# Performance work log

Measured on AMD Instinct MI355X. Metric: run time of the kernel, lower is better.

## Reference

```python
import jax, jax.numpy as jnp
import numpy as np

B, IN_DIM, HIDDEN, N_CLASSES, D_Z = 16384, 1024, 2048, 8, 256
LN_EPS = 1e-5  # torch.nn.LayerNorm default


def _l2_normalize(x, axis=1, eps=1e-12):
    # matches F.normalize: x / max(||x||, eps)
    n = jnp.sqrt(jnp.sum(x * x, axis=axis, keepdims=True))
    return x / jnp.maximum(n, eps)


def setup_inputs() -> dict:
    key = jax.random.key(0)
    ks = jax.random.split(key, 9)
    s1 = 1.0 / np.sqrt(IN_DIM)
    s2 = 1.0 / np.sqrt(HIDDEN)
    return {
        "feat": jax.random.normal(ks[0], (B, IN_DIM), dtype=jnp.float32),
        "z_cat": jax.random.normal(ks[1], (B, D_Z), dtype=jnp.float32),
        "mu_cat": jax.random.normal(ks[2], (N_CLASSES, D_Z), dtype=jnp.float32),
        "ln_gamma": jnp.ones((N_CLASSES, IN_DIM), dtype=jnp.float32),
        "ln_beta": jnp.zeros((N_CLASSES, IN_DIM), dtype=jnp.float32),
        "W1": jax.random.uniform(ks[3], (N_CLASSES, IN_DIM, HIDDEN), jnp.float32, -s1, s1),
        "b1": jax.random.uniform(ks[4], (N_CLASSES, HIDDEN), jnp.float32, -s1, s1),
        "W2": jax.random.uniform(ks[5], (N_CLASSES, HIDDEN, N_CLASSES), jnp.float32, -s2, s2),
        "b2": jax.random.uniform(ks[6], (N_CLASSES, N_CLASSES), jnp.float32, -s2, s2),
        "tau_gate": 1,
    }


def reference(feat, z_cat, mu_cat, ln_gamma, ln_beta, W1, b1, W2, b2, tau_gate):
    # --- cosine-similarity softmax gate ---
    zn = _l2_normalize(z_cat, axis=1)            # [B, Dz]
    mun = _l2_normalize(mu_cat, axis=1)          # [E, Dz]
    sims = zn @ mun.T                            # [B, E]
    tau = max(1e-6, float(tau_gate))
    w = jax.nn.softmax(sims / tau, axis=1)       # [B, E]

    # --- batched experts: LN -> Linear -> ReLU -> (Dropout=identity, eval) -> Linear ---
    mu = jnp.mean(feat, axis=-1, keepdims=True)
    var = jnp.mean(jnp.square(feat - mu), axis=-1, keepdims=True)
    xhat = (feat - mu) * jax.lax.rsqrt(var + LN_EPS)            # [B, D] (shared)
    x_e = xhat[None] * ln_gamma[:, None, :] + ln_beta[:, None, :]  # [E, B, D]
    h = jax.nn.relu(jnp.einsum('ebd,edh->ebh', x_e, W1) + b1[:, None, :])  # [E, B, H]
    exp_logits = jnp.einsum('ebh,ehc->ebc', h, W2) + b2[:, None, :]        # [E, B, C]

    # --- gate-weighted sum over experts ---
    logits = jnp.einsum('ebc,be->bc', exp_logits, w)  # [B, C]
    return logits, w
```

## Files before the change

kernel.cpp:

```cpp
#include <hip/hip_runtime.h>
#include <hip/hip_bf16.h>
#include <cstdint>

#define NB     16384
#define DIN    1024
#define HID    2048
#define NE     8
#define NC     8
#define DZ     256

#define BK2    32
#define NKT    (DIN / BK2)
#define GRID_MAIN 256

typedef short bf16x8 __attribute__((ext_vector_type(8)));
typedef float f32x4  __attribute__((ext_vector_type(4)));

__device__ __forceinline__ unsigned short f2bf(float f) {
    unsigned int u = __float_as_uint(f);
    unsigned int r = (u + 0x7FFFu + ((u >> 16) & 1u)) >> 16;
    return (unsigned short)r;
}

__device__ __forceinline__ void async_copy16(const void* g, void* l) {
    __builtin_amdgcn_global_load_lds(
        (const __attribute__((address_space(1))) unsigned int*)g,
        (__attribute__((address_space(3))) unsigned int*)l, 16, 0, 0);
}

__global__ __launch_bounds__(256) void k_gate(const float* __restrict__ z,
                                              const float* __restrict__ mu,
                                              const int* __restrict__ tau_i,
                                              const float* __restrict__ b2,
                                              float* __restrict__ wout,
                                              float* __restrict__ logits) {
    int row = blockIdx.x * 4 + (threadIdx.x >> 6);
    int l = threadIdx.x & 63;
    float4 zv = *(const float4*)&z[(size_t)row * DZ + l * 4];
    float zz = zv.x * zv.x + zv.y * zv.y + zv.z * zv.z + zv.w * zv.w;
    float dots[NE], mm[NE];
#pragma unroll
    for (int e = 0; e < NE; ++e) {
        float4 m = *(const float4*)&mu[e * DZ + l * 4];
        dots[e] = zv.x * m.x + zv.y * m.y + zv.z * m.z + zv.w * m.w;
        mm[e]   = m.x * m.x + m.y * m.y + m.z * m.z + m.w * m.w;
    }
#pragma unroll
    for (int off = 32; off; off >>= 1) {
        zz += __shfl_xor(zz, off);
#pragma unroll
        for (int e = 0; e < NE; ++e) {
            dots[e] += __shfl_xor(dots[e], off);
            mm[e]   += __shfl_xor(mm[e], off);
        }
    }
    float zn = fmaxf(sqrtf(zz), 1e-12f);
    float tau = fmaxf(1e-6f, (float)tau_i[0]);
    float s[NE], mx = -1e30f;
#pragma unroll
    for (int e = 0; e < NE; ++e) {
        s[e] = dots[e] / (zn * fmaxf(sqrtf(mm[e]), 1e-12f)) / tau;
        mx = fmaxf(mx, s[e]);
    }
    float sum = 0.f;
#pragma unroll
    for (int e = 0; e < NE; ++e) { s[e] = expf(s[e] - mx); sum += s[e]; }
    float inv = 1.f / sum;
    if (l < NE) {
        wout[(size_t)row * NE + l] = s[l] * inv;
        float acc = 0.f;
#pragma unroll
        for (int e = 0; e < NE; ++e) acc += s[e] * inv * b2[e * NC + l];
        logits[(size_t)row * NC + l] = acc;
    }
}

__global__ __launch_bounds__(256) void k_ln(const float* __restrict__ feat,
                                            unsigned short* __restrict__ xhat) {
    int row = blockIdx.x;
    int t = threadIdx.x;
    float4 v = *(const float4*)&feat[(size_t)row * DIN + t * 4];
    float s  = v.x + v.y + v.z + v.w;
    float sq = v.x * v.x + v.y * v.y + v.z * v.z + v.w * v.w;
#pragma unroll
    for (int off = 32; off; off >>= 1) {
        s  += __shfl_down(s, off);
        sq += __shfl_down(sq, off);
    }
    __shared__ float ls[8];
    int w = t >> 6, l = t & 63;
    if (l == 0) { ls[w] = s; ls[4 + w] = sq; }
    __syncthreads();
    s  = ls[0] + ls[1] + ls[2] + ls[3];
    sq = ls[4] + ls[5] + ls[6] + ls[7];
    float mean = s * (1.f / DIN);
    float var  = sq * (1.f / DIN) - mean * mean;
    float r = 1.0f / sqrtf(var + 1e-5f);
    uint2 p;
    p.x = (unsigned)f2bf((v.x - mean) * r) | ((unsigned)f2bf((v.y - mean) * r) << 16);
    p.y = (unsigned)f2bf((v.z - mean) * r) | ((unsigned)f2bf((v.w - mean) * r) << 16);
    *(uint2*)&xhat[(size_t)row * DIN + t * 4] = p;
}

__global__ __launch_bounds__(256) void k_w2prep(const float* __restrict__ W2,
                                                const float* __restrict__ b1,
                                                unsigned short* __restrict__ w2t,
                                                float* __restrict__ b1p) {
    int i = blockIdx.x * 256 + threadIdx.x;
    int e = i >> 15;
    int rem = i & 32767;
    int c = rem >> 11;
    int h = rem & 2047;
    float v = (c < NC) ? W2[((size_t)(e * HID + h)) * NC + c] : 0.f;
    w2t[i] = f2bf(v);
    if (i < NE * HID) b1p[i] = b1[i];
}

__global__ __launch_bounds__(256) void k_w1prep(const float* __restrict__ W1,
                                                const float* __restrict__ gamma,
                                                const float* __restrict__ beta,
                                                unsigned short* __restrict__ w1t,
                                                float* __restrict__ b1p) {
    __shared__ float tile[64][65];
    int e  = blockIdx.z;
    int d0 = blockIdx.y * 64;
    int h0 = blockIdx.x * 64;
    int tx = threadIdx.x & 15, ty = threadIdx.x >> 4;
#pragma unroll
    for (int rr = 0; rr < 4; ++rr) {
        int d = ty + rr * 16;
        float4 v = *(const float4*)&W1[((size_t)e * DIN + d0 + d) * HID + h0 + tx * 4];
        tile[tx * 4 + 0][d] = v.x;
        tile[tx * 4 + 1][d] = v.y;
        tile[tx * 4 + 2][d] = v.z;
        tile[tx * 4 + 3][d] = v.w;
    }
    __syncthreads();
    float4 g = *(const float4*)&gamma[(size_t)e * DIN + d0 + tx * 4];
#pragma unroll
    for (int rr = 0; rr < 4; ++rr) {
        int h = ty + rr * 16;
        uint2 p;
        p.x = (unsigned)f2bf(tile[h][tx * 4 + 0] * g.x) |
              ((unsigned)f2bf(tile[h][tx * 4 + 1] * g.y) << 16);
        p.y = (unsigned)f2bf(tile[h][tx * 4 + 2] * g.z) |
              ((unsigned)f2bf(tile[h][tx * 4 + 3] * g.w) << 16);
        *(uint2*)&w1t[((size_t)e * HID + h0 + h) * DIN + d0 + tx * 4] = p;
    }
    if (threadIdx.x < 64) {
        int h = threadIdx.x;
        float sacc = 0.f;
        for (int r = 0; r < 64; ++r)
            sacc += beta[(size_t)e * DIN + d0 + r] * tile[h][r];
        atomicAdd(&b1p[(size_t)e * HID + h0 + h], sacc);
    }
}


#define WAITV(n_) asm volatile("s_waitcnt vmcnt(" #n_ ")" ::: "memory")
#define BAR()  do { __builtin_amdgcn_s_barrier(); __builtin_amdgcn_sched_barrier(0); } while (0)

#define STAGE(tile_) do {                                                     \
    char* dst_ = (char*)lds + (((tile_) & 3) << 15) + (t << 4);               \
    const size_t ro_ = (size_t)srow * DIN + (size_t)(tile_) * BK2 + sk;       \
    async_copy16(gA + ro_, dst_);                                             \
    async_copy16(gA + ro_ + (size_t)128 * DIN, dst_ + 8192);                  \
    async_copy16(gB + ro_, dst_ + 16384);                                     \
    async_copy16(gB + ro_ + (size_t)128 * DIN, dst_ + 24576);                 \
} while (0)

#define KBODY(kt_) do {                                                       \
    const short* la_ = (const short*)(lds + (((kt_) & 3) << 15));             \
    const short* lb_ = la_ + 8192;                                            \
    bf16x8 bF_[4];                                                            \
    _Pragma("unroll")                                                         \
    for (int j_ = 0; j_ < 4; ++j_)                                            \
        bF_[j_] = *(const bf16x8*)&lb_[(wn + 16 * j_ + ml) * BK2 + cswz];     \
    __builtin_amdgcn_s_setprio(1);                                            \
    _Pragma("unroll")                                                         \
    for (int i_ = 0; i_ < 8; ++i_) {                                          \
        const bf16x8 aF_ = *(const bf16x8*)&la_[(wm + 16 * i_ + ml) * BK2 + cswz]; \
        _Pragma("unroll")                                                     \
        for (int j_ = 0; j_ < 4; ++j_)                                        \
            acc[i_][j_] = __builtin_amdgcn_mfma_f32_16x16x32_bf16(            \
                aF_, bF_[j_], acc[i_][j_], 0, 0, 0);                          \
    }                                                                         \
    __builtin_amdgcn_s_setprio(0);                                            \
} while (0)

__global__ __launch_bounds__(512, 2) void moe_main(
        const unsigned short* __restrict__ xhat,
        const unsigned short* __restrict__ w1t,
        const float* __restrict__ b1p,
        const unsigned short* __restrict__ w2t,
        const float* __restrict__ wg,
        float* __restrict__ logits) {
    __shared__ __align__(16) char lds[131072];

    const int t  = threadIdx.x;
    const int w  = t >> 6, l = t & 63;
    const int q  = l >> 4, ml = l & 15;
    const int wm = (w >> 2) * 128;
    const int wn = (w & 3) * 64;
    const int cswz = (q ^ ((ml >> 1) & 3)) * 8;
    const int srow = t >> 2;
    const int sk   = ((t & 3) ^ ((srow >> 1) & 3)) * 8;

    const int e    = blockIdx.x & 7;
    const int slot = blockIdx.x >> 3;
    char* myht = (char*)lds + w * 5120;

    for (int pr = 0; pr < 2; ++pr) {
        const int b0 = (pr * 32 + slot) * 256;
        const unsigned short* gB = xhat + (size_t)b0 * DIN;

        f32x4 acc2[4];
#pragma unroll
        for (int tb = 0; tb < 4; ++tb) acc2[tb] = (f32x4){0.f, 0.f, 0.f, 0.f};

        for (int ms = 0; ms < 8; ++ms) {
            const int hid0 = ms * 256;
            const unsigned short* gA = w1t + ((size_t)e * HID + hid0) * DIN;

            f32x4 acc[8][4];
#pragma unroll
            for (int i = 0; i < 8; ++i)
#pragma unroll
                for (int j = 0; j < 4; ++j) acc[i][j] = (f32x4){0.f, 0.f, 0.f, 0.f};

            STAGE(0); STAGE(1); STAGE(2);
#pragma unroll 1
            for (int kt = 0; kt < NKT - 3; ++kt) {
                WAITV(8);
                BAR();
                STAGE(kt + 3);
                KBODY(kt);
            }
            WAITV(8); BAR(); KBODY(29);
            WAITV(4); BAR(); KBODY(30);
            WAITV(0); BAR(); KBODY(31);

#pragma unroll
            for (int s = 0; s < 4; ++s) {
#pragma unroll
                for (int i2 = 0; i2 < 2; ++i2) {
                    const int i = 2 * s + i2;
                    const float4 bias = *(const float4*)
                        &b1p[(size_t)e * HID + hid0 + wm + 16 * i + 4 * q];
#pragma unroll
                    for (int j = 0; j < 4; ++j) {
                        float v0 = fmaxf(acc[i][j].x + bias.x, 0.f);
                        float v1 = fmaxf(acc[i][j].y + bias.y, 0.f);
                        float v2 = fmaxf(acc[i][j].z + bias.z, 0.f);
                        float v3 = fmaxf(acc[i][j].w + bias.w, 0.f);
                        uint2 p;
                        p.x = (unsigned)f2bf(v0) | ((unsigned)f2bf(v1) << 16);
                        p.y = (unsigned)f2bf(v2) | ((unsigned)f2bf(v3) << 16);
                        *(uint2*)(myht + (16 * j + ml) * 80 + (16 * i2 + 4 * q) * 2) = p;
                    }
                }
                const bf16x8 b2f = *(const bf16x8*)&w2t[((size_t)e * 16 + ml) * HID +
                                                        hid0 + wm + 32 * s + 8 * q];
#pragma unroll
                for (int tb = 0; tb < 4; ++tb) {
                    const bf16x8 a2f =
                        *(const bf16x8*)(myht + (16 * tb + ml) * 80 + q * 16);
                    acc2[tb] = __builtin_amdgcn_mfma_f32_16x16x32_bf16(
                        a2f, b2f, acc2[tb], 0, 0, 0);
                }
            }
            __syncthreads();
        }

        float* red = (float*)(lds + 65536);
        if (w >= 4) {
            float* dst = red + ((w & 3) * 64 + l) * 16;
#pragma unroll
            for (int tb = 0; tb < 4; ++tb)
#pragma unroll
                for (int r = 0; r < 4; ++r) dst[tb * 4 + r] = acc2[tb][r];
        }
        __syncthreads();
        if (w < 4) {
            const float* src = red + (w * 64 + l) * 16;
            if (ml < NC) {
#pragma unroll
                for (int tb = 0; tb < 4; ++tb) {
#pragma unroll
                    for (int r = 0; r < 4; ++r) {
                        float v = acc2[tb][r] + src[tb * 4 + r];
                        const int bg = b0 + wn + 16 * tb + 4 * q + r;
                        atomicAdd(&logits[(size_t)bg * NC + ml],
                                  wg[(size_t)bg * NE + e] * v);
                    }
                }
            }
        }
        __syncthreads();
    }
}

extern "C" void kernel_launch(void* const* d_in, const int* in_sizes, int n_in,
                              void* d_out, int out_size, void* d_ws, size_t ws_size,
                              hipStream_t stream) {
    const float* feat  = (const float*)d_in[0];
    const float* z     = (const float*)d_in[1];
    const float* mu    = (const float*)d_in[2];
    const float* gamma = (const float*)d_in[3];
    const float* beta  = (const float*)d_in[4];
    const float* W1    = (const float*)d_in[5];
    const float* b1    = (const float*)d_in[6];
    const float* W2    = (const float*)d_in[7];
    const float* b2    = (const float*)d_in[8];
    const int*   tau   = (const int*)d_in[9];

    float* logits = (float*)d_out;
    float* wout   = logits + (size_t)NB * NC;

    char* ws = (char*)d_ws;
    unsigned short* xhat = (unsigned short*)ws;
    unsigned short* w1t  = (unsigned short*)(ws + 33554432);
    unsigned short* w2t  = (unsigned short*)(ws + 67108864);
    float*          b1p  = (float*)(ws + 67633152);

    k_gate<<<NB / 4, 256, 0, stream>>>(z, mu, tau, b2, wout, logits);
    k_ln<<<NB, 256, 0, stream>>>(feat, xhat);
    k_w2prep<<<(NE * 16 * HID) / 256, 256, 0, stream>>>(W2, b1, w2t, b1p);
    k_w1prep<<<dim3(HID / 64, DIN / 64, NE), 256, 0, stream>>>(W1, gamma, beta, w1t, b1p);
    moe_main<<<dim3(GRID_MAIN), 512, 0, stream>>>(xhat, w1t, b1p, w2t, wout, logits);
}
```

Before: 723.2 us.

## Split GEMM k-iteration into two phases with interleaved staging and barriers

Each k-tile iteration of the main GEMM loop now runs as two halves. Each half loads four A fragments into registers, issues half of the next tile's async global-to-LDS copies (A in the first half, B in the second), passes a barrier, then runs 16 MFMAs. This spreads memory issue across the compute phases and keeps waves in lockstep, in the style of ping-pong scheduling. It adds two extra workgroup barriers per iteration, which may cost more than the overlap gains.

```diff
diff --git a/kernel.cpp b/kernel.cpp
--- a/kernel.cpp
+++ b/kernel.cpp
@@ -160,31 +160,53 @@
 #define WAITV(n_) asm volatile("s_waitcnt vmcnt(" #n_ ")" ::: "memory")
 #define BAR()  do { __builtin_amdgcn_s_barrier(); __builtin_amdgcn_sched_barrier(0); } while (0)
 
-#define STAGE(tile_) do {                                                     \
+#define STAGEA(tile_) do {                                                    \
     char* dst_ = (char*)lds + (((tile_) & 3) << 15) + (t << 4);               \
-    const size_t ro_ = (size_t)srow * DIN + (size_t)(tile_) * BK2 + sk;       \
+    const size_t ro_ = rowoff + (size_t)(tile_) * BK2;                        \
     async_copy16(gA + ro_, dst_);                                             \
     async_copy16(gA + ro_ + (size_t)128 * DIN, dst_ + 8192);                  \
-    async_copy16(gB + ro_, dst_ + 16384);                                     \
-    async_copy16(gB + ro_ + (size_t)128 * DIN, dst_ + 24576);                 \
 } while (0)
 
-#define KBODY(kt_) do {                                                       \
+#define STAGEB(tile_) do {                                                    \
+    char* dst_ = (char*)lds + (((tile_) & 3) << 15) + 16384 + (t << 4);       \
+    const size_t ro_ = rowoff + (size_t)(tile_) * BK2;                        \
+    async_copy16(gB + ro_, dst_);                                             \
+    async_copy16(gB + ro_ + (size_t)128 * DIN, dst_ + 8192);                  \
+} while (0)
+
+#define ITER(kt_, DO_STAGE) do {                                              \
     const short* la_ = (const short*)(lds + (((kt_) & 3) << 15));             \
     const short* lb_ = la_ + 8192;                                            \
-    bf16x8 bF_[4];                                                            \
+    bf16x8 bF_[4], aF_[4];                                                    \
     _Pragma("unroll")                                                         \
     for (int j_ = 0; j_ < 4; ++j_)                                            \
         bF_[j_] = *(const bf16x8*)&lb_[(wn + 16 * j_ + ml) * BK2 + cswz];     \
+    _Pragma("unroll")                                                         \
+    for (int i_ = 0; i_ < 4; ++i_)                                            \
+        aF_[i_] = *(const bf16x8*)&la_[(wm + 16 * i_ + ml) * BK2 + cswz];     \
+    if (DO_STAGE) STAGEA((kt_) + 3);                                          \
+    BAR();                                                                    \
     __builtin_amdgcn_s_setprio(1);                                            \
     _Pragma("unroll")                                                         \
-    for (int i_ = 0; i_ < 8; ++i_) {                                          \
-        const bf16x8 aF_ = *(const bf16x8*)&la_[(wm + 16 * i_ + ml) * BK2 + cswz]; \
+    for (int i_ = 0; i_ < 4; ++i_)                                            \
         _Pragma("unroll")                                                     \
         for (int j_ = 0; j_ < 4; ++j_)                                        \
             acc[i_][j_] = __builtin_amdgcn_mfma_f32_16x16x32_bf16(            \
-                aF_, bF_[j_], acc[i_][j_], 0, 0, 0);                          \
-    }                                                                         \
+                aF_[i_], bF_[j_], acc[i_][j_], 0, 0, 0);                      \
+    __builtin_amdgcn_s_setprio(0);                                            \
+    BAR();                                                                    \
+    _Pragma("unroll")                                                         \
+    for (int i_ = 0; i_ < 4; ++i_)                                            \
+        aF_[i_] = *(const bf16x8*)&la_[(wm + 64 + 16 * i_ + ml) * BK2 + cswz];\
+    if (DO_STAGE) STAGEB((kt_) + 3);                                          \
+    BAR();                                                                    \
+    __builtin_amdgcn_s_setprio(1);                                            \
+    _Pragma("unroll")                                                         \
+    for (int i_ = 0; i_ < 4; ++i_)                                            \
+        _Pragma("unroll")                                                     \
+        for (int j_ = 0; j_ < 4; ++j_)                                        \
+            acc[4 + i_][j_] = __builtin_amdgcn_mfma_f32_16x16x32_bf16(        \
+                aF_[i_], bF_[j_], acc[4 + i_][j_], 0, 0, 0);                  \
     __builtin_amdgcn_s_setprio(0);                                            \
 } while (0)
 
@@ -204,7 +226,8 @@
     const int wn = (w & 3) * 64;
     const int cswz = (q ^ ((ml >> 1) & 3)) * 8;
     const int srow = t >> 2;
-    const int sk   = ((t & 3) ^ ((srow >> 1) & 3)) * 8;
+    const size_t rowoff = (size_t)srow * DIN +
+                          (size_t)(((t & 3) ^ ((srow >> 1) & 3)) * 8);
 
     const int e    = blockIdx.x & 7;
     const int slot = blockIdx.x >> 3;
@@ -228,17 +251,18 @@
 #pragma unroll
                 for (int j = 0; j < 4; ++j) acc[i][j] = (f32x4){0.f, 0.f, 0.f, 0.f};
 
-            STAGE(0); STAGE(1); STAGE(2);
+            STAGEA(0); STAGEB(0);
+            STAGEA(1); STAGEB(1);
+            STAGEA(2); STAGEB(2);
 #pragma unroll 1
             for (int kt = 0; kt < NKT - 3; ++kt) {
                 WAITV(8);
                 BAR();
-                STAGE(kt + 3);
-                KBODY(kt);
+                ITER(kt, 1);
             }
-            WAITV(8); BAR(); KBODY(29);
-            WAITV(4); BAR(); KBODY(30);
-            WAITV(0); BAR(); KBODY(31);
+            WAITV(8); BAR(); ITER(29, 0);
+            WAITV(4); BAR(); ITER(30, 0);
+            WAITV(0); BAR(); ITER(31, 0);
 
 #pragma unroll
             for (int s = 0; s < 4; ++s) {
```

New measurement: 703.7 us. 2.7% less time.

## Load B operand directly to registers and double-buffer A tiles across stages

Applied to the files above, without the earlier changes.

The main GEMM loop stops staging xhat tiles through LDS. Each wave now loads its B fragments straight from global memory into registers, while only W1 tiles go through a two-slot LDS double buffer. Prefetch continues across ms and pr iterations, which removes the per-ms __syncthreads and shrinks LDS from 128KB to 72KB. In exchange, the pipeline depth drops from 4 stages to 2 with full vmcnt(0) waits, and B global loads become redundant across waves sharing columns, which may expose memory latency.

```diff
diff --git a/kernel.cpp b/kernel.cpp
--- a/kernel.cpp
+++ b/kernel.cpp
@@ -160,22 +160,23 @@
 #define WAITV(n_) asm volatile("s_waitcnt vmcnt(" #n_ ")" ::: "memory")
 #define BAR()  do { __builtin_amdgcn_s_barrier(); __builtin_amdgcn_sched_barrier(0); } while (0)
 
-#define STAGE(tile_) do {                                                     \
-    char* dst_ = (char*)lds + (((tile_) & 3) << 15) + (t << 4);               \
-    const size_t ro_ = (size_t)srow * DIN + (size_t)(tile_) * BK2 + sk;       \
-    async_copy16(gA + ro_, dst_);                                             \
-    async_copy16(gA + ro_ + (size_t)128 * DIN, dst_ + 8192);                  \
-    async_copy16(gB + ro_, dst_ + 16384);                                     \
-    async_copy16(gB + ro_ + (size_t)128 * DIN, dst_ + 24576);                 \
+#define ISSA(gAp_, kt_, b_) do {                                              \
+    char* d_ = ldsA + ((b_) << 14) + (t << 4);                                \
+    const size_t ro_ = aRowOff + (size_t)(kt_) * BK2;                         \
+    async_copy16((gAp_) + ro_, d_);                                          \
+    async_copy16((gAp_) + ro_ + (size_t)128 * DIN, d_ + 8192);               \
 } while (0)
 
-#define KBODY(kt_) do {                                                       \
-    const short* la_ = (const short*)(lds + (((kt_) & 3) << 15));             \
-    const short* lb_ = la_ + 8192;                                            \
-    bf16x8 bF_[4];                                                            \
-    _Pragma("unroll")                                                         \
-    for (int j_ = 0; j_ < 4; ++j_)                                            \
-        bF_[j_] = *(const bf16x8*)&lb_[(wn + 16 * j_ + ml) * BK2 + cswz];     \
+#define ISSB(set_, prn_, kt_) do {                                            \
+    const size_t po_ = (size_t)(prn_) * 8388608u + (size_t)(kt_) * BK2;       \
+    set_[0] = *(const bf16x8*)&xhat[bB0 + po_];                               \
+    set_[1] = *(const bf16x8*)&xhat[bB1 + po_];                               \
+    set_[2] = *(const bf16x8*)&xhat[bB2 + po_];                               \
+    set_[3] = *(const bf16x8*)&xhat[bB3 + po_];                               \
+} while (0)
+
+#define COMP(set_, b_) do {                                                   \
+    const short* la_ = (const short*)(ldsA + ((b_) << 14));                   \
     __builtin_amdgcn_s_setprio(1);                                            \
     _Pragma("unroll")                                                         \
     for (int i_ = 0; i_ < 8; ++i_) {                                          \
@@ -183,7 +184,7 @@
         _Pragma("unroll")                                                     \
         for (int j_ = 0; j_ < 4; ++j_)                                        \
             acc[i_][j_] = __builtin_amdgcn_mfma_f32_16x16x32_bf16(            \
-                aF_, bF_[j_], acc[i_][j_], 0, 0, 0);                          \
+                aF_, set_[j_], acc[i_][j_], 0, 0, 0);                         \
     }                                                                         \
     __builtin_amdgcn_s_setprio(0);                                            \
 } while (0)
@@ -195,7 +196,8 @@
         const unsigned short* __restrict__ w2t,
         const float* __restrict__ wg,
         float* __restrict__ logits) {
-    __shared__ __align__(16) char lds[131072];
+    __shared__ __align__(16) char lds[73728];
+    char* ldsA = (char*)lds;
 
     const int t  = threadIdx.x;
     const int w  = t >> 6, l = t & 63;
@@ -204,15 +206,30 @@
     const int wn = (w & 3) * 64;
     const int cswz = (q ^ ((ml >> 1) & 3)) * 8;
     const int srow = t >> 2;
-    const int sk   = ((t & 3) ^ ((srow >> 1) & 3)) * 8;
+    const size_t aRowOff = (size_t)srow * DIN +
+                           (size_t)(((t & 3) ^ ((srow >> 1) & 3)) * 8);
 
     const int e    = blockIdx.x & 7;
     const int slot = blockIdx.x >> 3;
-    char* myht = (char*)lds + w * 5120;
+    char* myht = (char*)lds + 32768 + w * 5120;
+
+    const size_t bB0 = (size_t)(slot * 256 + wn + 16 * 0 + ml) * DIN + q * 8;
+    const size_t bB1 = (size_t)(slot * 256 + wn + 16 * 1 + ml) * DIN + q * 8;
+    const size_t bB2 = (size_t)(slot * 256 + wn + 16 * 2 + ml) * DIN + q * 8;
+    const size_t bB3 = (size_t)(slot * 256 + wn + 16 * 3 + ml) * DIN + q * 8;
+
+    const unsigned short* eA = w1t + (size_t)e * HID * DIN;
+
+    bf16x8 bC[4], bN[4];
+
+    {
+        const unsigned short* gA0 = eA;
+        ISSA(gA0, 0, 0);
+        ISSB(bC, 0, 0);
+    }
 
     for (int pr = 0; pr < 2; ++pr) {
         const int b0 = (pr * 32 + slot) * 256;
-        const unsigned short* gB = xhat + (size_t)b0 * DIN;
 
         f32x4 acc2[4];
 #pragma unroll
@@ -220,7 +237,7 @@
 
         for (int ms = 0; ms < 8; ++ms) {
             const int hid0 = ms * 256;
-            const unsigned short* gA = w1t + ((size_t)e * HID + hid0) * DIN;
+            const unsigned short* gA = eA + (size_t)hid0 * DIN;
 
             f32x4 acc[8][4];
 #pragma unroll
@@ -228,17 +245,27 @@
 #pragma unroll
                 for (int j = 0; j < 4; ++j) acc[i][j] = (f32x4){0.f, 0.f, 0.f, 0.f};
 
-            STAGE(0); STAGE(1); STAGE(2);
 #pragma unroll 1
-            for (int kt = 0; kt < NKT - 3; ++kt) {
-                WAITV(8);
+            for (int kp = 0; kp < 16; ++kp) {
+                WAITV(0);
                 BAR();
-                STAGE(kt + 3);
-                KBODY(kt);
+                ISSA(gA, 2 * kp + 1, 1);
+                ISSB(bN, pr, 2 * kp + 1);
+                COMP(bC, 0);
+                WAITV(0);
+                BAR();
+                if (kp < 15) {
+                    ISSA(gA, 2 * kp + 2, 0);
+                    ISSB(bC, pr, 2 * kp + 2);
+                } else if (!(pr == 1 && ms == 7)) {
+                    const int msn = (ms + 1) & 7;
+                    const int prn = pr + (ms == 7 ? 1 : 0);
+                    const unsigned short* gAn = eA + (size_t)(msn * 256) * DIN;
+                    ISSA(gAn, 0, 0);
+                    ISSB(bC, prn, 0);
+                }
+                COMP(bN, 1);
             }
-            WAITV(8); BAR(); KBODY(29);
-            WAITV(4); BAR(); KBODY(30);
-            WAITV(0); BAR(); KBODY(31);
 
 #pragma unroll
             for (int s = 0; s < 4; ++s) {
@@ -269,10 +296,10 @@
                         a2f, b2f, acc2[tb], 0, 0, 0);
                 }
             }
-            __syncthreads();
         }
 
-        float* red = (float*)(lds + 65536);
+        __syncthreads();
+        float* red = (float*)(lds + 32768);
         if (w >= 4) {
             float* dst = red + ((w & 3) * 64 + l) * 16;
 #pragma unroll
@@ -296,7 +323,6 @@
                 }
             }
         }
-        __syncthreads();
     }
 }
 
```

Result: slower. 983.3 us (+36.0%).

## Double the GEMM K-tile, switch to double buffering with cross-tile prefetch, fuse gate and LayerNorm

Applied to the files above, without the earlier changes.

Raises the main GEMM K-tile from 32 to 64 and replaces the 4-deep pipeline with a 2-buffer scheme that waits for all loads each step. The first stage of the next hidden tile or next batch pass is issued before the last compute step, so the pipeline no longer drains between tiles. This is meant to cut barrier and pipeline-fill overhead, and the XOR swizzle is widened to 8 chunks for the larger tile. It also merges the gate and LayerNorm kernels into one launch and removes one end-of-pass barrier. The trade-off is less load latency hiding, because every iteration waits on vmcnt(0), and a larger LDS footprint.

```diff
diff --git a/kernel.cpp b/kernel.cpp
--- a/kernel.cpp
+++ b/kernel.cpp
@@ -9,7 +9,7 @@
 #define NC     8
 #define DZ     256
 
-#define BK2    32
+#define BK2    64
 #define NKT    (DIN / BK2)
 #define GRID_MAIN 256
 
@@ -28,78 +28,79 @@
         (__attribute__((address_space(3))) unsigned int*)l, 16, 0, 0);
 }
 
-__global__ __launch_bounds__(256) void k_gate(const float* __restrict__ z,
-                                              const float* __restrict__ mu,
-                                              const int* __restrict__ tau_i,
-                                              const float* __restrict__ b2,
-                                              float* __restrict__ wout,
-                                              float* __restrict__ logits) {
-    int row = blockIdx.x * 4 + (threadIdx.x >> 6);
-    int l = threadIdx.x & 63;
-    float4 zv = *(const float4*)&z[(size_t)row * DZ + l * 4];
-    float zz = zv.x * zv.x + zv.y * zv.y + zv.z * zv.z + zv.w * zv.w;
-    float dots[NE], mm[NE];
-#pragma unroll
-    for (int e = 0; e < NE; ++e) {
-        float4 m = *(const float4*)&mu[e * DZ + l * 4];
-        dots[e] = zv.x * m.x + zv.y * m.y + zv.z * m.z + zv.w * m.w;
-        mm[e]   = m.x * m.x + m.y * m.y + m.z * m.z + m.w * m.w;
-    }
-#pragma unroll
-    for (int off = 32; off; off >>= 1) {
-        zz += __shfl_xor(zz, off);
+__global__ __launch_bounds__(256) void k_pre(const float* __restrict__ feat,
+                                             unsigned short* __restrict__ xhat,
+                                             const float* __restrict__ z,
+                                             const float* __restrict__ mu,
+                                             const int* __restrict__ tau_i,
+                                             const float* __restrict__ b2,
+                                             float* __restrict__ wout,
+                                             float* __restrict__ logits) {
+    if (blockIdx.x < NB) {
+        int row = blockIdx.x;
+        int t = threadIdx.x;
+        float4 v = *(const float4*)&feat[(size_t)row * DIN + t * 4];
+        float s  = v.x + v.y + v.z + v.w;
+        float sq = v.x * v.x + v.y * v.y + v.z * v.z + v.w * v.w;
+#pragma unroll
+        for (int off = 32; off; off >>= 1) {
+            s  += __shfl_down(s, off);
+            sq += __shfl_down(sq, off);
+        }
+        __shared__ float ls[8];
+        int w = t >> 6, l = t & 63;
+        if (l == 0) { ls[w] = s; ls[4 + w] = sq; }
+        __syncthreads();
+        s  = ls[0] + ls[1] + ls[2] + ls[3];
+        sq = ls[4] + ls[5] + ls[6] + ls[7];
+        float mean = s * (1.f / DIN);
+        float var  = sq * (1.f / DIN) - mean * mean;
+        float r = 1.0f / sqrtf(var + 1e-5f);
+        uint2 p;
+        p.x = (unsigned)f2bf((v.x - mean) * r) | ((unsigned)f2bf((v.y - mean) * r) << 16);
+        p.y = (unsigned)f2bf((v.z - mean) * r) | ((unsigned)f2bf((v.w - mean) * r) << 16);
+        *(uint2*)&xhat[(size_t)row * DIN + t * 4] = p;
+    } else {
+        int row = (blockIdx.x - NB) * 4 + (threadIdx.x >> 6);
+        int l = threadIdx.x & 63;
+        float4 zv = *(const float4*)&z[(size_t)row * DZ + l * 4];
+        float zz = zv.x * zv.x + zv.y * zv.y + zv.z * zv.z + zv.w * zv.w;
+        float dots[NE], mm[NE];
 #pragma unroll
         for (int e = 0; e < NE; ++e) {
-            dots[e] += __shfl_xor(dots[e], off);
-            mm[e]   += __shfl_xor(mm[e], off);
-        }
-    }
-    float zn = fmaxf(sqrtf(zz), 1e-12f);
-    float tau = fmaxf(1e-6f, (float)tau_i[0]);
-    float s[NE], mx = -1e30f;
-#pragma unroll
-    for (int e = 0; e < NE; ++e) {
-        s[e] = dots[e] / (zn * fmaxf(sqrtf(mm[e]), 1e-12f)) / tau;
-        mx = fmaxf(mx, s[e]);
-    }
-    float sum = 0.f;
-#pragma unroll
-    for (int e = 0; e < NE; ++e) { s[e] = expf(s[e] - mx); sum += s[e]; }
-    float inv = 1.f / sum;
-    if (l < NE) {
-        wout[(size_t)row * NE + l] = s[l] * inv;
-        float acc = 0.f;
-#pragma unroll
-        for (int e = 0; e < NE; ++e) acc += s[e] * inv * b2[e * NC + l];
-        logits[(size_t)row * NC + l] = acc;
-    }
-}
-
-__global__ __launch_bounds__(256) void k_ln(const float* __restrict__ feat,
-                                            unsigned short* __restrict__ xhat) {
-    int row = blockIdx.x;
-    int t = threadIdx.x;
-    float4 v = *(const float4*)&feat[(size_t)row * DIN + t * 4];
-    float s  = v.x + v.y + v.z + v.w;
-    float sq = v.x * v.x + v.y * v.y + v.z * v.z + v.w * v.w;
-#pragma unroll
-    for (int off = 32; off; off >>= 1) {
-        s  += __shfl_down(s, off);
-        sq += __shfl_down(sq, off);
-    }
-    __shared__ float ls[8];
-    int w = t >> 6, l = t & 63;
-    if (l == 0) { ls[w] = s; ls[4 + w] = sq; }
-    __syncthreads();
-    s  = ls[0] + ls[1] + ls[2] + ls[3];
-    sq = ls[4] + ls[5] + ls[6] + ls[7];
-    float mean = s * (1.f / DIN);
-    float var  = sq * (1.f / DIN) - mean * mean;
-    float r = 1.0f / sqrtf(var + 1e-5f);
-    uint2 p;
-    p.x = (unsigned)f2bf((v.x - mean) * r) | ((unsigned)f2bf((v.y - mean) * r) << 16);
-    p.y = (unsigned)f2bf((v.z - mean) * r) | ((unsigned)f2bf((v.w - mean) * r) << 16);
-    *(uint2*)&xhat[(size_t)row * DIN + t * 4] = p;
+            float4 m = *(const float4*)&mu[e * DZ + l * 4];
+            dots[e] = zv.x * m.x + zv.y * m.y + zv.z * m.z + zv.w * m.w;
+            mm[e]   = m.x * m.x + m.y * m.y + m.z * m.z + m.w * m.w;
+        }
+#pragma unroll
+        for (int off = 32; off; off >>= 1) {
+            zz += __shfl_xor(zz, off);
+#pragma unroll
+            for (int e = 0; e < NE; ++e) {
+                dots[e] += __shfl_xor(dots[e], off);
+                mm[e]   += __shfl_xor(mm[e], off);
+            }
+        }
+        float zn = fmaxf(sqrtf(zz), 1e-12f);
+        float tau = fmaxf(1e-6f, (float)tau_i[0]);
+        float s[NE], mx = -1e30f;
+#pragma unroll
+        for (int e = 0; e < NE; ++e) {
+            s[e] = dots[e] / (zn * fmaxf(sqrtf(mm[e]), 1e-12f)) / tau;
+            mx = fmaxf(mx, s[e]);
+        }
+        float sum = 0.f;
+#pragma unroll
+        for (int e = 0; e < NE; ++e) { s[e] = expf(s[e] - mx); sum += s[e]; }
+        float inv = 1.f / sum;
+        if (l < NE) {
+            wout[(size_t)row * NE + l] = s[l] * inv;
+            float acc = 0.f;
+#pragma unroll
+            for (int e = 0; e < NE; ++e) acc += s[e] * inv * b2[e * NC + l];
+            logits[(size_t)row * NC + l] = acc;
+        }
+    }
 }
 
 __global__ __launch_bounds__(256) void k_w2prep(const float* __restrict__ W2,
@@ -160,32 +161,57 @@
 #define WAITV(n_) asm volatile("s_waitcnt vmcnt(" #n_ ")" ::: "memory")
 #define BAR()  do { __builtin_amdgcn_s_barrier(); __builtin_amdgcn_sched_barrier(0); } while (0)
 
-#define STAGE(tile_) do {                                                     \
-    char* dst_ = (char*)lds + (((tile_) & 3) << 15) + (t << 4);               \
-    const size_t ro_ = (size_t)srow * DIN + (size_t)(tile_) * BK2 + sk;       \
-    async_copy16(gA + ro_, dst_);                                             \
-    async_copy16(gA + ro_ + (size_t)128 * DIN, dst_ + 8192);                  \
-    async_copy16(gB + ro_, dst_ + 16384);                                     \
-    async_copy16(gB + ro_ + (size_t)128 * DIN, dst_ + 24576);                 \
+#define STAGE(gAp_, gBp_, kt64_, par_) do {                                   \
+    char* da_ = (char*)lds + ((par_) << 16) + (t << 4);                       \
+    const size_t ko_ = sbase + (size_t)(kt64_) * BK2;                         \
+    async_copy16((gAp_) + ko_,          da_);                                 \
+    async_copy16((gAp_) + ko_ + 65536,  da_ + 8192);                          \
+    async_copy16((gAp_) + ko_ + 131072, da_ + 16384);                         \
+    async_copy16((gAp_) + ko_ + 196608, da_ + 24576);                         \
+    async_copy16((gBp_) + ko_,          da_ + 32768);                         \
+    async_copy16((gBp_) + ko_ + 65536,  da_ + 40960);                         \
+    async_copy16((gBp_) + ko_ + 131072, da_ + 49152);                         \
+    async_copy16((gBp_) + ko_ + 196608, da_ + 57344);                         \
 } while (0)
 
-#define KBODY(kt_) do {                                                       \
-    const short* la_ = (const short*)(lds + (((kt_) & 3) << 15));             \
-    const short* lb_ = la_ + 8192;                                            \
-    bf16x8 bF_[4];                                                            \
-    _Pragma("unroll")                                                         \
-    for (int j_ = 0; j_ < 4; ++j_)                                            \
-        bF_[j_] = *(const bf16x8*)&lb_[(wn + 16 * j_ + ml) * BK2 + cswz];     \
-    __builtin_amdgcn_s_setprio(1);                                            \
-    _Pragma("unroll")                                                         \
-    for (int i_ = 0; i_ < 8; ++i_) {                                          \
-        const bf16x8 aF_ = *(const bf16x8*)&la_[(wm + 16 * i_ + ml) * BK2 + cswz]; \
+#define KBODY(par_) do {                                                      \
+    const short* la_ = (const short*)(lds + ((par_) << 16));                  \
+    const short* lb_ = la_ + 16384;                                           \
+    {                                                                         \
+        bf16x8 bF_[4];                                                        \
         _Pragma("unroll")                                                     \
         for (int j_ = 0; j_ < 4; ++j_)                                        \
-            acc[i_][j_] = __builtin_amdgcn_mfma_f32_16x16x32_bf16(            \
-                aF_, bF_[j_], acc[i_][j_], 0, 0, 0);                          \
+            bF_[j_] = *(const bf16x8*)&lb_[(wn + 16 * j_ + ml) * BK2 + csw0]; \
+        __builtin_amdgcn_s_setprio(1);                                        \
+        _Pragma("unroll")                                                     \
+        for (int i_ = 0; i_ < 8; ++i_) {                                      \
+            const bf16x8 aF_ =                                                \
+                *(const bf16x8*)&la_[(wm + 16 * i_ + ml) * BK2 + csw0];       \
+            _Pragma("unroll")                                                 \
+            for (int j_ = 0; j_ < 4; ++j_)                                    \
+                acc[i_][j_] = __builtin_amdgcn_mfma_f32_16x16x32_bf16(        \
+                    aF_, bF_[j_], acc[i_][j_], 0, 0, 0);                      \
+        }                                                                     \
+        __builtin_amdgcn_s_setprio(0);                                        \
     }                                                                         \
-    __builtin_amdgcn_s_setprio(0);                                            \
+    {                                                                         \
+        const int cs1_ = csw0 ^ 32;                                           \
+        bf16x8 bF_[4];                                                        \
+        _Pragma("unroll")                                                     \
+        for (int j_ = 0; j_ < 4; ++j_)                                        \
+            bF_[j_] = *(const bf16x8*)&lb_[(wn + 16 * j_ + ml) * BK2 + cs1_]; \
+        __builtin_amdgcn_s_setprio(1);                                        \
+        _Pragma("unroll")                                                     \
+        for (int i_ = 0; i_ < 8; ++i_) {                                      \
+            const bf16x8 aF_ =                                                \
+                *(const bf16x8*)&la_[(wm + 16 * i_ + ml) * BK2 + cs1_];       \
+            _Pragma("unroll")                                                 \
+            for (int j_ = 0; j_ < 4; ++j_)                                    \
+                acc[i_][j_] = __builtin_amdgcn_mfma_f32_16x16x32_bf16(        \
+                    aF_, bF_[j_], acc[i_][j_], 0, 0, 0);                      \
+        }                                                                     \
+        __builtin_amdgcn_s_setprio(0);                                        \
+    }                                                                         \
 } while (0)
 
 __global__ __launch_bounds__(512, 2) void moe_main(
@@ -202,13 +228,16 @@
     const int q  = l >> 4, ml = l & 15;
     const int wm = (w >> 2) * 128;
     const int wn = (w & 3) * 64;
-    const int cswz = (q ^ ((ml >> 1) & 3)) * 8;
-    const int srow = t >> 2;
-    const int sk   = ((t & 3) ^ ((srow >> 1) & 3)) * 8;
+    const int csw0 = (q ^ (ml & 7)) * 8;
+    const size_t sbase = (size_t)(t >> 3) * DIN +
+                         (size_t)(((t & 7) ^ ((t >> 3) & 7)) * 8);
 
     const int e    = blockIdx.x & 7;
     const int slot = blockIdx.x >> 3;
-    char* myht = (char*)lds + w * 5120;
+    char* myht = (char*)lds + 65536 + w * 5120;
+    const unsigned short* eA = w1t + (size_t)e * HID * DIN;
+
+    STAGE(eA, xhat + (size_t)slot * 256 * DIN, 0, 0);
 
     for (int pr = 0; pr < 2; ++pr) {
         const int b0 = (pr * 32 + slot) * 256;
@@ -220,7 +249,7 @@
 
         for (int ms = 0; ms < 8; ++ms) {
             const int hid0 = ms * 256;
-            const unsigned short* gA = w1t + ((size_t)e * HID + hid0) * DIN;
+            const unsigned short* gA = eA + (size_t)hid0 * DIN;
 
             f32x4 acc[8][4];
 #pragma unroll
@@ -228,17 +257,22 @@
 #pragma unroll
                 for (int j = 0; j < 4; ++j) acc[i][j] = (f32x4){0.f, 0.f, 0.f, 0.f};
 
-            STAGE(0); STAGE(1); STAGE(2);
 #pragma unroll 1
-            for (int kt = 0; kt < NKT - 3; ++kt) {
-                WAITV(8);
+            for (int kt = 0; kt < NKT - 1; ++kt) {
+                WAITV(0);
                 BAR();
-                STAGE(kt + 3);
-                KBODY(kt);
-            }
-            WAITV(8); BAR(); KBODY(29);
-            WAITV(4); BAR(); KBODY(30);
-            WAITV(0); BAR(); KBODY(31);
+                STAGE(gA, gB, kt + 1, (kt + 1) & 1);
+                KBODY(kt & 1);
+            }
+            WAITV(0);
+            BAR();
+            if (!(pr == 1 && ms == 7)) {
+                const unsigned short* gAn = (ms == 7) ? eA : gA + (size_t)256 * DIN;
+                const unsigned short* gBn = (ms == 7) ? gB + (size_t)8192 * DIN : gB;
+                STAGE(gAn, gBn, 0, 0);
+            }
+            KBODY(1);
+            BAR();
 
 #pragma unroll
             for (int s = 0; s < 4; ++s) {
@@ -269,10 +303,10 @@
                         a2f, b2f, acc2[tb], 0, 0, 0);
                 }
             }
-            __syncthreads();
-        }
-
-        float* red = (float*)(lds + 65536);
+        }
+
+        __syncthreads();
+        float* red = (float*)(lds + 106496);
         if (w >= 4) {
             float* dst = red + ((w & 3) * 64 + l) * 16;
 #pragma unroll
@@ -296,7 +330,6 @@
                 }
             }
         }
-        __syncthreads();
     }
 }
 
@@ -323,8 +356,7 @@
     unsigned short* w2t  = (unsigned short*)(ws + 67108864);
     float*          b1p  = (float*)(ws + 67633152);
 
-    k_gate<<<NB / 4, 256, 0, stream>>>(z, mu, tau, b2, wout, logits);
-    k_ln<<<NB, 256, 0, stream>>>(feat, xhat);
+    k_pre<<<NB + NB / 4, 256, 0, stream>>>(feat, xhat, z, mu, tau, b2, wout, logits);
     k_w2prep<<<(NE * 16 * HID) / 256, 256, 0, stream>>>(W2, b1, w2t, b1p);
     k_w1prep<<<dim3(HID / 64, DIN / 64, NE), 256, 0, stream>>>(W1, gamma, beta, w1t, b1p);
     moe_main<<<dim3(GRID_MAIN), 512, 0, stream>>>(xhat, w1t, b1p, w2t, wout, logits);
```

Result: faster. 692.3 us (-4.3%).
